# Kernel optimization log

Measured on AMD Instinct MI355X. Metric: run time of the kernel, lower is better.

Reference implementation:

```python
import jax, jax.numpy as jnp
import numpy as np

EPS = 1e-5
GROUPS = 32


def _group_norm(x, w, b):
    # x: [B, C, H, W]
    B, C, H, W = x.shape
    xg = x.reshape(B, GROUPS, (C // GROUPS) * H * W)
    mean = xg.mean(axis=-1, keepdims=True)
    var = xg.var(axis=-1, keepdims=True)
    xn = ((xg - mean) * jax.lax.rsqrt(var + EPS)).reshape(B, C, H, W)
    return xn * w[None, :, None, None] + b[None, :, None, None]


def setup_inputs() -> dict:
    key = jax.random.key(0)
    ks = jax.random.split(key, 8)
    B, C, H, W = 2, 512, 64, 64
    s = 1.0 / np.sqrt(C)
    return {
        "hidden_states": jax.random.normal(ks[0], (B, C, H, W), jnp.float32),
        "gn_weight": jnp.ones((C,), jnp.float32),
        "gn_bias": jnp.zeros((C,), jnp.float32),
        "wq": jax.random.normal(ks[1], (C, C), jnp.float32) * s,
        "bq": jnp.zeros((C,), jnp.float32),
        "wk": jax.random.normal(ks[2], (C, C), jnp.float32) * s,
        "bk": jnp.zeros((C,), jnp.float32),
        "wv": jax.random.normal(ks[3], (C, C), jnp.float32) * s,
        "bv": jnp.zeros((C,), jnp.float32),
        "wo": jax.random.normal(ks[4], (C, C), jnp.float32) * s,
        "bo": jnp.zeros((C,), jnp.float32),
    }


def reference(hidden_states, gn_weight, gn_bias, wq, bq, wk, bk, wv, bv, wo, bo):
    x = hidden_states
    B, C, H, W = x.shape
    residual = x
    h = _group_norm(x, gn_weight, gn_bias)
    # [B, S, C] with S = H*W
    h = h.reshape(B, C, H * W).transpose(0, 2, 1)
    scale = jnp.asarray(C, h.dtype) ** -0.5
    q = (h @ wq.T + bq) * scale          # [B, S, C]
    k = h @ wk.T + bk                    # [B, S, C]
    v = h @ wv.T + bv                    # [B, S, C]
    attn = jax.nn.softmax(jnp.einsum("bsc,btc->bst", q, k), axis=-1)
    o = jnp.einsum("bst,btc->bsc", attn, v)
    o = o @ wo.T + bo
    o = o.transpose(0, 2, 1).reshape(B, C, H, W)
    return o + residual
```

## Files before the change

### kernel.cpp

```cpp
#include <hip/hip_runtime.h>
#include <hip/hip_bf16.h>
#include <stdint.h>

#define S_LEN 4096
#define C_DIM 512
#define NGROUPS 32
#define EPS_GN 1e-5f
#define QSCALE 0.044194173824159216f

typedef float f32x4 __attribute__((ext_vector_type(4)));
typedef float f32x16 __attribute__((ext_vector_type(16)));
typedef __bf16 bf16x8 __attribute__((ext_vector_type(8)));
typedef unsigned short u16;
typedef unsigned int u32;

__device__ __forceinline__ u16 f2bf(float f) {
    union { float f; u32 u; } v; v.f = f;
    u32 r = v.u + 0x7FFFu + ((v.u >> 16) & 1u);
    return (u16)(r >> 16);
}
__device__ __forceinline__ u32 pack2(float a, float b) {
    return (u32)f2bf(a) | ((u32)f2bf(b) << 16);
}

__device__ __forceinline__ void async16(const void* g, void* l) {
    __builtin_amdgcn_global_load_lds((const __attribute__((address_space(1))) u32*)g,
                                     (__attribute__((address_space(3))) u32*)l, 16, 0, 0);
}

#define BARRIER() do { asm volatile("" ::: "memory"); __builtin_amdgcn_s_barrier(); asm volatile("" ::: "memory"); } while (0)
#define WAIT_LGKM0() asm volatile("s_waitcnt lgkmcnt(0)" ::: "memory")
#define WAIT_VM0()   asm volatile("s_waitcnt vmcnt(0)" ::: "memory")

__global__ __launch_bounds__(256) void gn_stats_kernel(const float* __restrict__ x,
                                                       float* __restrict__ stats) {
    const int bg = blockIdx.x;
    const float* p = x + (size_t)bg * (16 * S_LEN);
    const int tid = threadIdx.x;
    float s = 0.f, ss = 0.f;
    for (int i = tid; i < (16 * S_LEN) / 4; i += 256) {
        const float4 v = ((const float4*)p)[i];
        s += v.x + v.y + v.z + v.w;
        ss += v.x * v.x + v.y * v.y + v.z * v.z + v.w * v.w;
    }
#pragma unroll
    for (int off = 32; off > 0; off >>= 1) {
        s += __shfl_down(s, off);
        ss += __shfl_down(ss, off);
    }
    __shared__ float rs_[4], rss_[4];
    if ((tid & 63) == 0) { rs_[tid >> 6] = s; rss_[tid >> 6] = ss; }
    __syncthreads();
    if (tid == 0) {
        const float S = rs_[0] + rs_[1] + rs_[2] + rs_[3];
        const float SS = rss_[0] + rss_[1] + rss_[2] + rss_[3];
        const float mean = S * (1.f / 65536.f);
        const float var = SS * (1.f / 65536.f) - mean * mean;
        stats[bg * 2] = mean;
        stats[bg * 2 + 1] = rsqrtf(var + EPS_GN);
    }
}

__global__ __launch_bounds__(256) void wconv_kernel(const float* __restrict__ wq,
                                                    const float* __restrict__ wk,
                                                    const float* __restrict__ wv,
                                                    const float* __restrict__ wo,
                                                    u16* __restrict__ wb) {
    const int i = blockIdx.x * 256 + threadIdx.x;
    const int m = i >> 16;
    const int j = i & 65535;
    const float* src = (m == 0) ? wq : (m == 1) ? wk : (m == 2) ? wv : wo;
    const float4 v = ((const float4*)src)[j];
    ushort4 o;
    o.x = f2bf(v.x); o.y = f2bf(v.y); o.z = f2bf(v.z); o.w = f2bf(v.w);
    ((ushort4*)wb)[i] = o;
}

__global__ __launch_bounds__(256) void hnorm_kernel(const float* __restrict__ x,
                                                    const float* __restrict__ stats,
                                                    const float* __restrict__ gw,
                                                    const float* __restrict__ gb,
                                                    u16* __restrict__ h) {
    __shared__ float tile[32][65];
    const int b = blockIdx.z, c0 = blockIdx.y * 32, s0 = blockIdx.x * 64;
    const int tid = threadIdx.x;
#pragma unroll
    for (int kq = 0; kq < 2; ++kq) {
        const int f = tid + kq * 256;
        const int c = f >> 4, cs = f & 15;
        const float4 v = *(const float4*)(x + ((size_t)(b * C_DIM + c0 + c) * S_LEN + s0 + cs * 4));
        const int g = (c0 + c) >> 4;
        const float mean = stats[(b * NGROUPS + g) * 2];
        const float rstd = stats[(b * NGROUPS + g) * 2 + 1];
        const float a = rstd * gw[c0 + c];
        const float be = gb[c0 + c] - mean * a;
        tile[c][cs * 4 + 0] = v.x * a + be;
        tile[c][cs * 4 + 1] = v.y * a + be;
        tile[c][cs * 4 + 2] = v.z * a + be;
        tile[c][cs * 4 + 3] = v.w * a + be;
    }
    __syncthreads();
#pragma unroll
    for (int kq = 0; kq < 2; ++kq) {
        const int f = tid + kq * 256;
        const int s = f >> 3, c4 = f & 7;
        ushort4 o;
        o.x = f2bf(tile[c4 * 4 + 0][s]);
        o.y = f2bf(tile[c4 * 4 + 1][s]);
        o.z = f2bf(tile[c4 * 4 + 2][s]);
        o.w = f2bf(tile[c4 * 4 + 3][s]);
        *(ushort4*)(h + ((size_t)(b * S_LEN + s0 + s) * C_DIM + c0 + c4 * 4)) = o;
    }
}

template <int MODE>
__global__ __launch_bounds__(256) void proj_kernel(
    const u16* __restrict__ A, const u16* __restrict__ W,
    const float* __restrict__ bias0, const float* __restrict__ bias1,
    const float* __restrict__ bias2,
    u16* __restrict__ oq, u16* __restrict__ ok_, u16* __restrict__ ovT,
    const float* __restrict__ xres, float* __restrict__ out) {
    __shared__ u16 As[128 * 64];
    __shared__ u16 Bs[128 * 64];

    const int mt = blockIdx.x;
    const int nt = blockIdx.y;
    const int m0 = mt * 128;
    const int which = (MODE == 0) ? (nt >> 2) : 0;
    const int n0 = (MODE == 0) ? ((nt & 3) * 128) : (nt * 128);

    const u16* Ab = A + (size_t)m0 * C_DIM;
    const u16* Bb = W + (size_t)which * (C_DIM * C_DIM) + (size_t)n0 * C_DIM;

    const int tid = threadIdx.x;
    const int w = tid >> 6, l = tid & 63, lr = l & 15, lg = l >> 4;
    const int wr = (w >> 1) * 64, wc = (w & 1) * 64;

    f32x4 acc[4][4];
#pragma unroll
    for (int i = 0; i < 4; ++i)
#pragma unroll
        for (int j = 0; j < 4; ++j) acc[i][j] = (f32x4){0.f, 0.f, 0.f, 0.f};

    for (int ks = 0; ks < 8; ++ks) {
        const int k0 = ks * 64;
#pragma unroll
        for (int i = 0; i < 4; ++i) {
            const int ch = w * 4 + i;
            const int row = ch * 8 + (l >> 3);
            const int sp = (l & 7) ^ (row & 7);
            async16(Ab + (size_t)row * C_DIM + k0 + sp * 8, (void*)(As + ch * 512));
            async16(Bb + (size_t)row * C_DIM + k0 + sp * 8, (void*)(Bs + ch * 512));
        }
        asm volatile("s_waitcnt vmcnt(0)" ::: "memory");
        __syncthreads();
#pragma unroll
        for (int kk = 0; kk < 2; ++kk) {
            bf16x8 af[4], bfr[4];
#pragma unroll
            for (int i = 0; i < 4; ++i) {
                const int row = wr + i * 16 + lr;
                const int p = (kk * 4 + lg) ^ (row & 7);
                af[i] = *(const bf16x8*)(As + row * 64 + p * 8);
            }
#pragma unroll
            for (int j = 0; j < 4; ++j) {
                const int row = wc + j * 16 + lr;
                const int p = (kk * 4 + lg) ^ (row & 7);
                bfr[j] = *(const bf16x8*)(Bs + row * 64 + p * 8);
            }
#pragma unroll
            for (int i = 0; i < 4; ++i)
#pragma unroll
                for (int j = 0; j < 4; ++j)
                    acc[i][j] = __builtin_amdgcn_mfma_f32_16x16x32_bf16(af[i], bfr[j], acc[i][j], 0, 0, 0);
        }
        __syncthreads();
    }

    const float* bias = (MODE == 0) ? (which == 0 ? bias0 : (which == 1 ? bias1 : bias2)) : bias0;
#pragma unroll
    for (int j = 0; j < 4; ++j) {
        const int gc = n0 + wc + j * 16 + lr;
        const float bv = bias[gc];
#pragma unroll
        for (int i = 0; i < 4; ++i) {
            const int gr0 = m0 + wr + i * 16 + lg * 4;
#pragma unroll
            for (int r = 0; r < 4; ++r) {
                const int gr = gr0 + r;
                const float v = acc[i][j][r] + bv;
                if (MODE == 0) {
                    if (which == 0)
                        oq[(size_t)gr * C_DIM + gc] = f2bf(v * QSCALE);
                    else if (which == 1)
                        ok_[(size_t)gr * C_DIM + gc] = f2bf(v);
                    else
                        ovT[((size_t)(gr >> 12) * C_DIM + gc) * S_LEN + (gr & (S_LEN - 1))] = f2bf(v);
                } else {
                    const size_t idx = ((size_t)(gr >> 12) * C_DIM + gc) * S_LEN + (gr & (S_LEN - 1));
                    out[idx] = v + xres[idx];
                }
            }
        }
    }
}

__global__ __launch_bounds__(512, 2) void flash_kernel(
    const u16* __restrict__ q, const u16* __restrict__ k, const u16* __restrict__ vT,
    u16* __restrict__ opart, float* __restrict__ ml) {
    __shared__ u16 LDSU[81920];
    float* const Sx = (float*)(LDSU + 65536);

    const int bid = blockIdx.x;
    const int wgid = (bid & 7) * 32 + (bid >> 3);
    const int qt = wgid & 31;
    const int sp = (wgid >> 5) & 3;
    const int b = wgid >> 7;
    const int m0 = qt * 128;
    const int tbeg = sp * 1024;

    const int tid = threadIdx.x;
    const int w = tid >> 6;
    const int l = tid & 63;
    const int rg = w >> 1;
    const int h = w & 1;
    const int ln = l & 31;
    const int hi = l >> 5;

    bf16x8 qf[16];
    {
        const u16* qrow = q + ((size_t)(b * S_LEN) + m0 + rg * 32 + ln) * C_DIM + h * 256 + hi * 8;
#pragma unroll
        for (int cc = 0; cc < 16; ++cc)
            qf[cc] = *(const bf16x8*)(qrow + cc * 16);
    }

    f32x16 oacc[8];
#pragma unroll
    for (int dt = 0; dt < 8; ++dt)
#pragma unroll
        for (int r = 0; r < 16; ++r) oacc[dt][r] = 0.f;
    float rm = -3.0e38f, rl = 0.f;

    const u16* kbase = k + (size_t)b * S_LEN * C_DIM;
    const u16* vbase = vT + (size_t)b * C_DIM * S_LEN;

#pragma unroll
    for (int i = 0; i < 4; ++i) {
        const int row = w * 4 + i;
        async16(kbase + (size_t)(tbeg + row) * C_DIM + ((l ^ (row & 7)) * 8),
                (void*)(LDSU + row * 512));
    }
#pragma unroll
    for (int i = 0; i < 4; ++i) {
        const int ch = w * 4 + i;
        const int d0 = ch * 16;
        const int d = d0 + (l >> 2);
        const int g = (l & 3) ^ ((d >> 1) & 3);
        async16(vbase + (size_t)d * S_LEN + tbeg + g * 8, (void*)(LDSU + 32768 + d0 * 32));
    }
    WAIT_VM0();
    BARRIER();

    for (int step = 0; step < 32; ++step) {
        const int t0 = tbeg + step * 32;
        const u16* kcur = LDSU + (step & 1) * 16384;
        const u16* vcur = LDSU + 32768 + (step & 1) * 16384;

        if (step < 31) {
            u16* knxt = LDSU + ((step + 1) & 1) * 16384;
#pragma unroll
            for (int i = 0; i < 4; ++i) {
                const int row = w * 4 + i;
                async16(kbase + (size_t)(t0 + 32 + row) * C_DIM + ((l ^ (row & 7)) * 8),
                        (void*)(knxt + row * 512));
            }
        }

        f32x16 sa;
#pragma unroll
        for (int r = 0; r < 16; ++r) sa[r] = 0.f;
        __builtin_amdgcn_s_setprio(1);
#pragma unroll
        for (int cc = 0; cc < 16; ++cc) {
            const int g = h * 32 + cc * 2 + hi;
            const bf16x8 af = *(const bf16x8*)(kcur + ln * 512 + ((g ^ (ln & 7)) * 8));
            sa = __builtin_amdgcn_mfma_f32_32x32x16_bf16(af, qf[cc], sa, 0, 0, 0);
        }
        __builtin_amdgcn_s_setprio(0);

        {
            float* swb = Sx + w * 1024 + l * 4;
#pragma unroll
            for (int c = 0; c < 4; ++c)
                *(f32x4*)(swb + c * 256) = (f32x4){sa[c * 4 + 0], sa[c * 4 + 1], sa[c * 4 + 2], sa[c * 4 + 3]};
            if (step < 31) { asm volatile("s_waitcnt vmcnt(4) lgkmcnt(0)" ::: "memory"); }
            else           { asm volatile("s_waitcnt vmcnt(0) lgkmcnt(0)" ::: "memory"); }
            BARRIER();
            const float* prb = Sx + (w ^ 1) * 1024 + l * 4;
#pragma unroll
            for (int c = 0; c < 4; ++c) {
                const f32x4 pv = *(const f32x4*)(prb + c * 256);
                sa[c * 4 + 0] += pv[0];
                sa[c * 4 + 1] += pv[1];
                sa[c * 4 + 2] += pv[2];
                sa[c * 4 + 3] += pv[3];
            }
        }

        if (step < 31) {
            u16* vnxt = LDSU + 32768 + ((step + 1) & 1) * 16384;
#pragma unroll
            for (int i = 0; i < 4; ++i) {
                const int ch = w * 4 + i;
                const int d0 = ch * 16;
                const int d = d0 + (l >> 2);
                const int g = (l & 3) ^ ((d >> 1) & 3);
                async16(vbase + (size_t)d * S_LEN + t0 + 32 + g * 8, (void*)(vnxt + d0 * 32));
            }
        }

        float t8[8];
#pragma unroll
        for (int r = 0; r < 8; ++r) t8[r] = fmaxf(sa[r], sa[r + 8]);
#pragma unroll
        for (int r = 0; r < 4; ++r) t8[r] = fmaxf(t8[r], t8[r + 4]);
        float pm = fmaxf(fmaxf(t8[0], t8[1]), fmaxf(t8[2], t8[3]));
        pm = fmaxf(pm, __shfl_xor(pm, 32));
        if (!__all(pm <= rm + 8.f)) {
            const float mn = fmaxf(rm, pm);
            const float al = __expf(rm - mn);
            rl *= al;
#pragma unroll
            for (int dt = 0; dt < 8; ++dt)
#pragma unroll
                for (int r = 0; r < 16; ++r) oacc[dt][r] *= al;
            rm = mn;
        }
#pragma unroll
        for (int r = 0; r < 16; ++r) sa[r] = __expf(sa[r] - rm);
        {
            float s8[8];
#pragma unroll
            for (int r = 0; r < 8; ++r) s8[r] = sa[r] + sa[r + 8];
#pragma unroll
            for (int r = 0; r < 4; ++r) s8[r] += s8[r + 4];
            float rs = (s8[0] + s8[1]) + (s8[2] + s8[3]);
            rs += __shfl_xor(rs, 32);
            rl += rs;
        }

        u32 wv[8], pw[8];
#pragma unroll
        for (int s4 = 0; s4 < 4; ++s4) {
            asm("v_cvt_pk_bf16_f32 %0, %1, %2" : "=v"(wv[s4 * 2 + 0]) : "v"(sa[s4 * 4 + 0]), "v"(sa[s4 * 4 + 1]));
            asm("v_cvt_pk_bf16_f32 %0, %1, %2" : "=v"(wv[s4 * 2 + 1]) : "v"(sa[s4 * 4 + 2]), "v"(sa[s4 * 4 + 3]));
        }
#pragma unroll
        for (int j = 0; j < 8; ++j) pw[j] = __shfl_xor((int)wv[j], 32);
        union { u32 u[4]; bf16x8 v; } pb0, pb1;
        pb0.u[0] = hi ? pw[2] : wv[0];
        pb0.u[1] = hi ? pw[3] : wv[1];
        pb0.u[2] = hi ? wv[2] : pw[0];
        pb0.u[3] = hi ? wv[3] : pw[1];
        pb1.u[0] = hi ? pw[6] : wv[4];
        pb1.u[1] = hi ? pw[7] : wv[5];
        pb1.u[2] = hi ? wv[6] : pw[4];
        pb1.u[3] = hi ? wv[7] : pw[5];

        __builtin_amdgcn_s_setprio(1);
#pragma unroll
        for (int dt = 0; dt < 8; ++dt) {
            const int d = h * 256 + dt * 32 + ln;
#pragma unroll
            for (int kk = 0; kk < 2; ++kk) {
                const int slot = (kk * 2 + hi) ^ ((d >> 1) & 3);
                const bf16x8 vf = *(const bf16x8*)(vcur + d * 32 + slot * 8);
                oacc[dt] = __builtin_amdgcn_mfma_f32_32x32x16_bf16(vf, kk ? pb1.v : pb0.v, oacc[dt], 0, 0, 0);
            }
        }
        __builtin_amdgcn_s_setprio(0);

        asm volatile("s_waitcnt vmcnt(4) lgkmcnt(0)" ::: "memory");
        BARRIER();
    }

    const float inv = 1.f / rl;
    u16* const Ot = LDSU;
    {
        const int qq = rg * 32 + ln;
#pragma unroll
        for (int dt = 0; dt < 8; ++dt) {
#pragma unroll
            for (int u = 0; u < 8; ++u) {
                const int d = h * 256 + dt * 32 + (((2 * u) & 3) + 8 * (u >> 1) + 4 * hi);
                const u32 word = pack2(oacc[dt][2 * u] * inv, oacc[dt][2 * u + 1] * inv);
                const int byte = qq * 1024 + ((d * 2) ^ ((qq & 7) << 4));
                *(u32*)((char*)Ot + byte) = word;
            }
        }
    }
    if (h == 0 && hi == 0) {
        float* mlp = ml + (size_t)((b * 4 + sp) * 2) * S_LEN;
        mlp[m0 + rg * 32 + ln] = rm;
        mlp[S_LEN + m0 + rg * 32 + ln] = rl;
    }
    WAIT_LGKM0();
    BARRIER();
    {
        u16* od = opart + ((size_t)((b * 4 + sp) * S_LEN) + m0) * C_DIM;
#pragma unroll
        for (int i = 0; i < 16; ++i) {
            const int qq = w * 16 + i;
            const int byte = qq * 1024 + ((l * 16) ^ ((qq & 7) << 4));
            const uint4 tv = *(const uint4*)((char*)Ot + byte);
            *(uint4*)(od + (size_t)qq * C_DIM + l * 8) = tv;
        }
    }
}

__global__ __launch_bounds__(256) void merge_kernel(const u16* __restrict__ opart,
                                                    const float* __restrict__ ml,
                                                    u16* __restrict__ o) {
    const int row = blockIdx.x;
    const int b = row >> 12, s = row & 4095;
    float mi[4], li[4];
#pragma unroll
    for (int i = 0; i < 4; ++i) {
        const float* mlp = ml + (size_t)((b * 4 + i) * 2) * S_LEN;
        mi[i] = mlp[s];
        li[i] = mlp[S_LEN + s];
    }
    float mm = fmaxf(fmaxf(mi[0], mi[1]), fmaxf(mi[2], mi[3]));
    float wsum = 0.f, wi[4];
#pragma unroll
    for (int i = 0; i < 4; ++i) { wi[i] = __expf(mi[i] - mm) * li[i]; wsum += wi[i]; }
    const float invw = 1.f / wsum;
#pragma unroll
    for (int i = 0; i < 4; ++i) wi[i] *= invw;

    const int c = threadIdx.x * 2;
    float a0 = 0.f, a1 = 0.f;
#pragma unroll
    for (int i = 0; i < 4; ++i) {
        const u16* p = opart + ((size_t)((b * 4 + i) * S_LEN) + s) * C_DIM + c;
        const ushort2 uu = *(const ushort2*)p;
        union { u32 u; float f; } c0, c1;
        c0.u = (u32)uu.x << 16; c1.u = (u32)uu.y << 16;
        a0 += wi[i] * c0.f;
        a1 += wi[i] * c1.f;
    }
    u16* orow = o + (size_t)row * C_DIM;
    ushort2 ov;
    ov.x = f2bf(a0); ov.y = f2bf(a1);
    *(ushort2*)(orow + c) = ov;
}

__global__ void sentinel_kernel(float* out) {
    if (threadIdx.x == 0 && blockIdx.x == 0) out[0] = 12345.0f;
}

extern "C" void kernel_launch(void* const* d_in, const int* in_sizes, int n_in,
                              void* d_out, int out_size, void* d_ws, size_t ws_size,
                              hipStream_t stream) {
    (void)in_sizes; (void)n_in; (void)out_size;
    const float* x  = (const float*)d_in[0];
    const float* gw = (const float*)d_in[1];
    const float* gb = (const float*)d_in[2];
    const float* wq = (const float*)d_in[3];
    const float* bq = (const float*)d_in[4];
    const float* wk = (const float*)d_in[5];
    const float* bk = (const float*)d_in[6];
    const float* wv = (const float*)d_in[7];
    const float* bv = (const float*)d_in[8];
    const float* wo = (const float*)d_in[9];
    const float* bo = (const float*)d_in[10];
    float* out = (float*)d_out;

    const size_t REQ = 69469184;
    if (ws_size < REQ) {
        sentinel_kernel<<<1, 64, 0, stream>>>(out);
        return;
    }
    char* ws = (char*)d_ws;
    float* stats = (float*)ws;
    u16* wb  = (u16*)(ws + 1024);
    u16* h   = (u16*)(ws + 1024 + 2097152);
    u16* qb  = h + (size_t)8192 * 512;
    u16* kb  = qb + (size_t)8192 * 512;
    u16* vTb = kb + (size_t)8192 * 512;
    u16* opart = vTb + (size_t)8192 * 512;
    float* ml = (float*)((char*)opart + (size_t)33554432);
    u16* ob = h;

    gn_stats_kernel<<<64, 256, 0, stream>>>(x, stats);
    wconv_kernel<<<1024, 256, 0, stream>>>(wq, wk, wv, wo, wb);
    hnorm_kernel<<<dim3(64, 16, 2), 256, 0, stream>>>(x, stats, gw, gb, h);
    proj_kernel<0><<<dim3(64, 12), 256, 0, stream>>>(h, wb, bq, bk, bv, qb, kb, vTb,
                                                     nullptr, nullptr);
    flash_kernel<<<256, 512, 0, stream>>>(qb, kb, vTb, opart, ml);
    merge_kernel<<<8192, 256, 0, stream>>>(opart, ml, ob);
    proj_kernel<1><<<dim3(64, 4), 256, 0, stream>>>(ob, wb + (size_t)3 * 262144, bo, nullptr,
                                                    nullptr, nullptr, nullptr, nullptr, x, out);
}
```

Baseline: 198.7 us.

## Software-pipeline softmax and PV of previous tile with QK of current tile

Restructures the attention inner loop so the softmax and P·V MFMAs for tile t-1 run between the QK MFMAs of tile t and the cross-wave score exchange. V tile loads move one iteration later, with adjusted vmcnt waits and an epilogue that finishes the last tile. The aim is to hide barrier latency and the softmax's exp and shuffle work behind MFMA work. It adds register pressure (sa, pb0 and pb1 stay live across iterations) and relies on more intricate wait-count bookkeeping.

```diff
diff --git a/kernel.cpp b/kernel.cpp
--- a/kernel.cpp
+++ b/kernel.cpp
@@ -252,24 +252,74 @@
         async16(kbase + (size_t)(tbeg + row) * C_DIM + ((l ^ (row & 7)) * 8),
                 (void*)(LDSU + row * 512));
     }
-#pragma unroll
-    for (int i = 0; i < 4; ++i) {
-        const int ch = w * 4 + i;
-        const int d0 = ch * 16;
-        const int d = d0 + (l >> 2);
-        const int g = (l & 3) ^ ((d >> 1) & 3);
-        async16(vbase + (size_t)d * S_LEN + tbeg + g * 8, (void*)(LDSU + 32768 + d0 * 32));
-    }
     WAIT_VM0();
     BARRIER();
 
-    for (int step = 0; step < 32; ++step) {
-        const int t0 = tbeg + step * 32;
-        const u16* kcur = LDSU + (step & 1) * 16384;
-        const u16* vcur = LDSU + 32768 + (step & 1) * 16384;
-
-        if (step < 31) {
-            u16* knxt = LDSU + ((step + 1) & 1) * 16384;
+    f32x16 sa;
+    union { u32 u[4]; bf16x8 v; } pb0, pb1;
+
+#define SOFTMAX_PACK()                                                                  \
+    do {                                                                                \
+        float t8[8];                                                                    \
+        _Pragma("unroll") for (int r = 0; r < 8; ++r) t8[r] = fmaxf(sa[r], sa[r + 8]);  \
+        _Pragma("unroll") for (int r = 0; r < 4; ++r) t8[r] = fmaxf(t8[r], t8[r + 4]);  \
+        float pm = fmaxf(fmaxf(t8[0], t8[1]), fmaxf(t8[2], t8[3]));                     \
+        pm = fmaxf(pm, __shfl_xor(pm, 32));                                             \
+        if (!__all(pm <= rm + 8.f)) {                                                   \
+            const float mn = fmaxf(rm, pm);                                             \
+            const float al = __expf(rm - mn);                                           \
+            rl *= al;                                                                   \
+            _Pragma("unroll") for (int dt = 0; dt < 8; ++dt)                            \
+                _Pragma("unroll") for (int r = 0; r < 16; ++r) oacc[dt][r] *= al;       \
+            rm = mn;                                                                    \
+        }                                                                               \
+        _Pragma("unroll") for (int r = 0; r < 16; ++r) sa[r] = __expf(sa[r] - rm);      \
+        {                                                                               \
+            float s8[8];                                                                \
+            _Pragma("unroll") for (int r = 0; r < 8; ++r) s8[r] = sa[r] + sa[r + 8];    \
+            _Pragma("unroll") for (int r = 0; r < 4; ++r) s8[r] += s8[r + 4];           \
+            float rs = (s8[0] + s8[1]) + (s8[2] + s8[3]);                               \
+            rs += __shfl_xor(rs, 32);                                                   \
+            rl += rs;                                                                   \
+        }                                                                               \
+        u32 wv[8], pw[8];                                                               \
+        _Pragma("unroll") for (int s4 = 0; s4 < 4; ++s4) {                              \
+            asm("v_cvt_pk_bf16_f32 %0, %1, %2" : "=v"(wv[s4 * 2 + 0])                   \
+                : "v"(sa[s4 * 4 + 0]), "v"(sa[s4 * 4 + 1]));                            \
+            asm("v_cvt_pk_bf16_f32 %0, %1, %2" : "=v"(wv[s4 * 2 + 1])                   \
+                : "v"(sa[s4 * 4 + 2]), "v"(sa[s4 * 4 + 3]));                            \
+        }                                                                               \
+        _Pragma("unroll") for (int j = 0; j < 8; ++j) pw[j] = __shfl_xor((int)wv[j], 32); \
+        pb0.u[0] = hi ? pw[2] : wv[0];                                                  \
+        pb0.u[1] = hi ? pw[3] : wv[1];                                                  \
+        pb0.u[2] = hi ? wv[2] : pw[0];                                                  \
+        pb0.u[3] = hi ? wv[3] : pw[1];                                                  \
+        pb1.u[0] = hi ? pw[6] : wv[4];                                                  \
+        pb1.u[1] = hi ? pw[7] : wv[5];                                                  \
+        pb1.u[2] = hi ? wv[6] : pw[4];                                                  \
+        pb1.u[3] = hi ? wv[7] : pw[5];                                                  \
+    } while (0)
+
+#define PV_BLOCK(VBUF)                                                                  \
+    do {                                                                                \
+        __builtin_amdgcn_s_setprio(1);                                                  \
+        _Pragma("unroll") for (int dt = 0; dt < 8; ++dt) {                              \
+            const int d = h * 256 + dt * 32 + ln;                                       \
+            _Pragma("unroll") for (int kk = 0; kk < 2; ++kk) {                          \
+                const int slot = (kk * 2 + hi) ^ ((d >> 1) & 3);                        \
+                const bf16x8 vf = *(const bf16x8*)((VBUF) + d * 32 + slot * 8);         \
+                oacc[dt] = __builtin_amdgcn_mfma_f32_32x32x16_bf16(                     \
+                    vf, kk ? pb1.v : pb0.v, oacc[dt], 0, 0, 0);                         \
+            }                                                                           \
+        }                                                                               \
+        __builtin_amdgcn_s_setprio(0);                                                  \
+    } while (0)
+
+    for (int t = 0; t < 32; ++t) {
+        const int t0 = tbeg + t * 32;
+
+        if (t < 31) {
+            u16* knxt = LDSU + ((t + 1) & 1) * 16384;
 #pragma unroll
             for (int i = 0; i < 4; ++i) {
                 const int row = w * 4 + i;
@@ -277,27 +327,51 @@
                         (void*)(knxt + row * 512));
             }
         }
-
-        f32x16 sa;
-#pragma unroll
-        for (int r = 0; r < 16; ++r) sa[r] = 0.f;
-        __builtin_amdgcn_s_setprio(1);
-#pragma unroll
-        for (int cc = 0; cc < 16; ++cc) {
-            const int g = h * 32 + cc * 2 + hi;
-            const bf16x8 af = *(const bf16x8*)(kcur + ln * 512 + ((g ^ (ln & 7)) * 8));
-            sa = __builtin_amdgcn_mfma_f32_32x32x16_bf16(af, qf[cc], sa, 0, 0, 0);
-        }
-        __builtin_amdgcn_s_setprio(0);
+        {
+            u16* vbuf = LDSU + 32768 + (t & 1) * 16384;
+#pragma unroll
+            for (int i = 0; i < 4; ++i) {
+                const int ch = w * 4 + i;
+                const int d0 = ch * 16;
+                const int d = d0 + (l >> 2);
+                const int g = (l & 3) ^ ((d >> 1) & 3);
+                async16(vbase + (size_t)d * S_LEN + t0 + g * 8, (void*)(vbuf + d0 * 32));
+            }
+        }
+
+        if (t) SOFTMAX_PACK();
+
+        {
+            const u16* kcur = LDSU + (t & 1) * 16384;
+#pragma unroll
+            for (int r = 0; r < 16; ++r) sa[r] = 0.f;
+            __builtin_amdgcn_s_setprio(1);
+#pragma unroll
+            for (int cc = 0; cc < 16; ++cc) {
+                const int g = h * 32 + cc * 2 + hi;
+                const bf16x8 af = *(const bf16x8*)(kcur + ln * 512 + ((g ^ (ln & 7)) * 8));
+                sa = __builtin_amdgcn_mfma_f32_32x32x16_bf16(af, qf[cc], sa, 0, 0, 0);
+            }
+            __builtin_amdgcn_s_setprio(0);
+        }
 
         {
             float* swb = Sx + w * 1024 + l * 4;
 #pragma unroll
             for (int c = 0; c < 4; ++c)
                 *(f32x4*)(swb + c * 256) = (f32x4){sa[c * 4 + 0], sa[c * 4 + 1], sa[c * 4 + 2], sa[c * 4 + 3]};
-            if (step < 31) { asm volatile("s_waitcnt vmcnt(4) lgkmcnt(0)" ::: "memory"); }
-            else           { asm volatile("s_waitcnt vmcnt(0) lgkmcnt(0)" ::: "memory"); }
-            BARRIER();
+        }
+
+        if (t < 31) { asm volatile("s_waitcnt vmcnt(8) lgkmcnt(0)" ::: "memory"); }
+        else        { asm volatile("s_waitcnt vmcnt(4) lgkmcnt(0)" ::: "memory"); }
+        BARRIER();
+
+        if (t) {
+            const u16* vprev = LDSU + 32768 + ((t - 1) & 1) * 16384;
+            PV_BLOCK(vprev);
+        }
+
+        {
             const float* prb = Sx + (w ^ 1) * 1024 + l * 4;
 #pragma unroll
             for (int c = 0; c < 4; ++c) {
@@ -309,82 +383,18 @@
             }
         }
 
-        if (step < 31) {
-            u16* vnxt = LDSU + 32768 + ((step + 1) & 1) * 16384;
-#pragma unroll
-            for (int i = 0; i < 4; ++i) {
-                const int ch = w * 4 + i;
-                const int d0 = ch * 16;
-                const int d = d0 + (l >> 2);
-                const int g = (l & 3) ^ ((d >> 1) & 3);
-                async16(vbase + (size_t)d * S_LEN + t0 + 32 + g * 8, (void*)(vnxt + d0 * 32));
-            }
-        }
-
-        float t8[8];
-#pragma unroll
-        for (int r = 0; r < 8; ++r) t8[r] = fmaxf(sa[r], sa[r + 8]);
-#pragma unroll
-        for (int r = 0; r < 4; ++r) t8[r] = fmaxf(t8[r], t8[r + 4]);
-        float pm = fmaxf(fmaxf(t8[0], t8[1]), fmaxf(t8[2], t8[3]));
-        pm = fmaxf(pm, __shfl_xor(pm, 32));
-        if (!__all(pm <= rm + 8.f)) {
-            const float mn = fmaxf(rm, pm);
-            const float al = __expf(rm - mn);
-            rl *= al;
-#pragma unroll
-            for (int dt = 0; dt < 8; ++dt)
-#pragma unroll
-                for (int r = 0; r < 16; ++r) oacc[dt][r] *= al;
-            rm = mn;
-        }
-#pragma unroll
-        for (int r = 0; r < 16; ++r) sa[r] = __expf(sa[r] - rm);
-        {
-            float s8[8];
-#pragma unroll
-            for (int r = 0; r < 8; ++r) s8[r] = sa[r] + sa[r + 8];
-#pragma unroll
-            for (int r = 0; r < 4; ++r) s8[r] += s8[r + 4];
-            float rs = (s8[0] + s8[1]) + (s8[2] + s8[3]);
-            rs += __shfl_xor(rs, 32);
-            rl += rs;
-        }
-
-        u32 wv[8], pw[8];
-#pragma unroll
-        for (int s4 = 0; s4 < 4; ++s4) {
-            asm("v_cvt_pk_bf16_f32 %0, %1, %2" : "=v"(wv[s4 * 2 + 0]) : "v"(sa[s4 * 4 + 0]), "v"(sa[s4 * 4 + 1]));
-            asm("v_cvt_pk_bf16_f32 %0, %1, %2" : "=v"(wv[s4 * 2 + 1]) : "v"(sa[s4 * 4 + 2]), "v"(sa[s4 * 4 + 3]));
-        }
-#pragma unroll
-        for (int j = 0; j < 8; ++j) pw[j] = __shfl_xor((int)wv[j], 32);
-        union { u32 u[4]; bf16x8 v; } pb0, pb1;
-        pb0.u[0] = hi ? pw[2] : wv[0];
-        pb0.u[1] = hi ? pw[3] : wv[1];
-        pb0.u[2] = hi ? wv[2] : pw[0];
-        pb0.u[3] = hi ? wv[3] : pw[1];
-        pb1.u[0] = hi ? pw[6] : wv[4];
-        pb1.u[1] = hi ? pw[7] : wv[5];
-        pb1.u[2] = hi ? wv[6] : pw[4];
-        pb1.u[3] = hi ? wv[7] : pw[5];
-
-        __builtin_amdgcn_s_setprio(1);
-#pragma unroll
-        for (int dt = 0; dt < 8; ++dt) {
-            const int d = h * 256 + dt * 32 + ln;
-#pragma unroll
-            for (int kk = 0; kk < 2; ++kk) {
-                const int slot = (kk * 2 + hi) ^ ((d >> 1) & 3);
-                const bf16x8 vf = *(const bf16x8*)(vcur + d * 32 + slot * 8);
-                oacc[dt] = __builtin_amdgcn_mfma_f32_32x32x16_bf16(vf, kk ? pb1.v : pb0.v, oacc[dt], 0, 0, 0);
-            }
-        }
-        __builtin_amdgcn_s_setprio(0);
-
-        asm volatile("s_waitcnt vmcnt(4) lgkmcnt(0)" ::: "memory");
+        if (t < 31) { asm volatile("s_waitcnt vmcnt(4) lgkmcnt(0)" ::: "memory"); }
+        else        { asm volatile("s_waitcnt vmcnt(0) lgkmcnt(0)" ::: "memory"); }
         BARRIER();
     }
+
+    SOFTMAX_PACK();
+    {
+        const u16* vprev = LDSU + 32768 + 16384;
+        PV_BLOCK(vprev);
+    }
+    WAIT_LGKM0();
+    BARRIER();
 
     const float inv = 1.f / rl;
     u16* const Ot = LDSU;
@@ -418,6 +428,8 @@
             *(uint4*)(od + (size_t)qq * C_DIM + l * 8) = tv;
         }
     }
+#undef SOFTMAX_PACK
+#undef PV_BLOCK
 }
 
 __global__ __launch_bounds__(256) void merge_kernel(const u16* __restrict__ opart,
```

Result: no change. 201.1 us (+1.2%).
